# Performance work log

Measured on AMD Instinct MI355X. Metric: run time of the kernel, lower is better.

## Reference

```python
import jax, jax.numpy as jnp
import numpy as np

B, S, D_MODEL, D_K, D_V, H = 2, 2048, 1024, 1024, 1024, 16


def setup_inputs() -> dict:
    key = jax.random.key(0)
    ks = jax.random.split(key, 12)
    s = 0.02
    inp = {
        "queries": jax.random.normal(ks[0], (B, S, D_MODEL), jnp.float32),
        "keys": jax.random.normal(ks[1], (B, S, D_MODEL), jnp.float32),
        "values": jax.random.normal(ks[2], (B, S, D_MODEL), jnp.float32),
        # causal mask: 1 where attention is disallowed (added as -1e9*mask)
        "mask": jnp.triu(jnp.ones((1, 1, S, S), jnp.float32), k=1),
        "Wq": jax.random.normal(ks[3], (D_MODEL, D_K), jnp.float32) * s,
        "bq": jnp.zeros((D_K,), jnp.float32),
        "Wk": jax.random.normal(ks[4], (D_MODEL, D_K), jnp.float32) * s,
        "bk": jnp.zeros((D_K,), jnp.float32),
        "Wv": jax.random.normal(ks[5], (D_MODEL, D_V), jnp.float32) * s,
        "bv": jnp.zeros((D_V,), jnp.float32),
        "Wo": jax.random.normal(ks[6], (D_K, D_MODEL), jnp.float32) * s,
        "bo": jnp.zeros((D_MODEL,), jnp.float32),
    }
    return inp


def _split_heads(x):  # [B,S,D] -> [B,H,S,D/H]
    b, s, d = x.shape
    return x.reshape(b, s, H, d // H).transpose(0, 2, 1, 3)


def reference(queries, keys, values, mask, Wq, bq, Wk, bk, Wv, bv, Wo, bo):
    q = _split_heads(queries @ Wq + bq)   # [B,H,S,hd]
    k = _split_heads(keys @ Wk + bk)
    v = _split_heads(values @ Wv + bv)
    # NOTE: original scales by sqrt(full d_k), not per-head dim (faithful quirk)
    scores = jnp.einsum("bhqd,bhkd->bhqk", q, k) / jnp.sqrt(jnp.float32(D_K))
    scores = scores + (-1e9) * mask
    w = jax.nn.softmax(scores, axis=-1)
    out = jnp.einsum("bhqk,bhkd->bhqd", w, v)        # [B,H,S,hd]
    out = out.transpose(0, 2, 1, 3).reshape(q.shape[0], q.shape[2], D_K)
    return out @ Wo + bo
```

## Files before the change

### kernel.cpp

```cpp
#include <hip/hip_runtime.h>
#include <hip/hip_bf16.h>
#include <cstdint>

typedef __bf16 bf16;
typedef __bf16 bf16x2 __attribute__((ext_vector_type(2)));
typedef __bf16 bf16x4 __attribute__((ext_vector_type(4)));
typedef __bf16 bf16x8 __attribute__((ext_vector_type(8)));
typedef float f32x4 __attribute__((ext_vector_type(4)));
typedef float f32x16 __attribute__((ext_vector_type(16)));
typedef unsigned int u32;

#define B_ 2
#define S_ 2048
#define DM 1024
#define H_ 16
#define HD 64

__device__ __forceinline__ void gload_lds16(const bf16* g, bf16* l) {
  __builtin_amdgcn_global_load_lds((const __attribute__((address_space(1))) void*)g,
                                   (__attribute__((address_space(3))) void*)l,
                                   16, 0, 0);
}

__device__ __forceinline__ u32 cvt_pk_bf16(float lo, float hi) {
  u32 r;
  asm("v_cvt_pk_bf16_f32 %0, %1, %2" : "=v"(r) : "v"(lo), "v"(hi));
  return r;
}

__global__ __launch_bounds__(256) void convert_k(const float* __restrict__ s0,
                                                 const float* __restrict__ s1,
                                                 const float* __restrict__ s2,
                                                 bf16* __restrict__ d0,
                                                 bf16* __restrict__ d1,
                                                 bf16* __restrict__ d2) {
  const float* s = (blockIdx.z == 0) ? s0 : (blockIdx.z == 1) ? s1 : s2;
  bf16* d = (blockIdx.z == 0) ? d0 : (blockIdx.z == 1) ? d1 : d2;
  const size_t i = ((size_t)blockIdx.x * 256 + threadIdx.x) * 8;
  f32x4 a = *(const f32x4*)(s + i);
  f32x4 b = *(const f32x4*)(s + i + 4);
  bf16x8 o;
#pragma unroll
  for (int j = 0; j < 4; j++) { o[j] = (bf16)a[j]; o[j + 4] = (bf16)b[j]; }
  *(bf16x8*)(d + i) = o;
}

__global__ __launch_bounds__(256) void transposeW_k(
    const float* __restrict__ w0, const float* __restrict__ w1,
    const float* __restrict__ w2, const float* __restrict__ w3,
    bf16* __restrict__ t0, bf16* __restrict__ t1,
    bf16* __restrict__ t2, bf16* __restrict__ t3) {
  const float* src = (blockIdx.z == 0) ? w0 : (blockIdx.z == 1) ? w1
                     : (blockIdx.z == 2) ? w2 : w3;
  bf16* dst = (blockIdx.z == 0) ? t0 : (blockIdx.z == 1) ? t1
              : (blockIdx.z == 2) ? t2 : t3;
  __shared__ float tile[32][33];
  const int tx = threadIdx.x, ty = threadIdx.y;
  const int x0 = blockIdx.x * 32, y0 = blockIdx.y * 32;
#pragma unroll
  for (int r = 0; r < 4; r++)
    tile[ty + r * 8][tx] = src[(size_t)(y0 + ty + r * 8) * DM + x0 + tx];
  __syncthreads();
#pragma unroll
  for (int r = 0; r < 4; r++)
    dst[(size_t)(x0 + ty + r * 8) * DM + y0 + tx] = (bf16)tile[tx][ty + r * 8];
}

struct GArgs { const void* A; const bf16* Bt; const float* bias; void* C; };
struct GArgs3 { GArgs g[3]; };

__global__ __launch_bounds__(512, 1) void gemm128_k(GArgs3 args, int M, int N,
                                                    int K) {
  __shared__ __align__(16) bf16 SA_[73728];
  bf16* const SB_ = SA_ + 24576;

  const int nwg = gridDim.x;
  const int id = blockIdx.x;
  const int wgid = (id & 7) * (nwg >> 3) + (id >> 3);
  const int z = wgid >> 7;
  const int rem = wgid & 127;
  const int tx = rem >> 5, ty = rem & 31;
  const GArgs ga = args.g[z];
  const int m0 = ty * 128, n0 = tx * 256;

  const int tid = threadIdx.x;
  const int lane = tid & 63, w = tid >> 6;
  const int l15 = lane & 15, q = lane >> 4;
  const int wr = w >> 2, wc = w & 3;

  const bf16* gA[2];
  const bf16* gB[4];
  int dA[2], dB[4];
#pragma unroll
  for (int i = 0; i < 2; i++) {
    const int ci = i * 512 + w * 64 + lane;
    const int row = ci >> 3, sc = (ci & 7) ^ (row & 7);
    gA[i] = (const bf16*)ga.A + (size_t)(m0 + row) * K + sc * 8;
    dA[i] = (i * 512 + w * 64) * 8;
  }
#pragma unroll
  for (int i = 0; i < 4; i++) {
    const int ci = i * 512 + w * 64 + lane;
    const int row = ci >> 3, sc = (ci & 7) ^ (row & 7);
    gB[i] = ga.Bt + (size_t)(n0 + row) * K + sc * 8;
    dB[i] = (i * 512 + w * 64) * 8;
  }

  const int cA0 = (q ^ (l15 & 7)) * 8;
  const int cA1 = ((4 + q) ^ (l15 & 7)) * 8;

  f32x4 acc[4][4] = {};

  const int NT = K >> 6;

#pragma unroll
  for (int tt = 0; tt < 2; tt++) {
    bf16* Ab = SA_ + tt * 8192;
    bf16* Bb = SB_ + tt * 16384;
    const int k0 = tt * 64;
    gload_lds16(gA[0] + k0, Ab + dA[0]);
    gload_lds16(gA[1] + k0, Ab + dA[1]);
#pragma unroll
    for (int i = 0; i < 4; i++) gload_lds16(gB[i] + k0, Bb + dB[i]);
  }
  asm volatile("s_waitcnt vmcnt(6)" ::: "memory");
  __builtin_amdgcn_s_barrier();

  for (int t = 0; t < NT; ++t) {
    const int rb = t % 3;
    const int wb = (t + 2) % 3;
    const int kpre = ((t + 2 < NT) ? t + 2 : NT - 1) << 6;
    {
      bf16* Ab = SA_ + wb * 8192;
      bf16* Bb = SB_ + wb * 16384;
      gload_lds16(gA[0] + kpre, Ab + dA[0]);
      gload_lds16(gA[1] + kpre, Ab + dA[1]);
#pragma unroll
      for (int i = 0; i < 4; i++) gload_lds16(gB[i] + kpre, Bb + dB[i]);
    }

    const bf16* Ab = SA_ + rb * 8192;
    const bf16* Bb = SB_ + rb * 16384;
    bf16x8 a[4][2], b[4][2];
#pragma unroll
    for (int mt = 0; mt < 4; mt++) {
      const int ro = (wr * 64 + mt * 16 + l15) * 64;
      a[mt][0] = *(const bf16x8*)(Ab + ro + cA0);
      a[mt][1] = *(const bf16x8*)(Ab + ro + cA1);
    }
#pragma unroll
    for (int nt = 0; nt < 4; nt++) {
      const int ro = (wc * 64 + nt * 16 + l15) * 64;
      b[nt][0] = *(const bf16x8*)(Bb + ro + cA0);
      b[nt][1] = *(const bf16x8*)(Bb + ro + cA1);
    }

    __builtin_amdgcn_s_setprio(1);
#pragma unroll
    for (int mt = 0; mt < 4; mt++)
#pragma unroll
      for (int nt = 0; nt < 4; nt++)
#pragma unroll
        for (int kk = 0; kk < 2; kk++)
          acc[mt][nt] = __builtin_amdgcn_mfma_f32_16x16x32_bf16(
              a[mt][kk], b[nt][kk], acc[mt][nt], 0, 0, 0);
    __builtin_amdgcn_s_setprio(0);

    asm volatile("s_waitcnt vmcnt(6)" ::: "memory");
    __builtin_amdgcn_s_barrier();
  }

  asm volatile("s_waitcnt vmcnt(0)" ::: "memory");
  __builtin_amdgcn_s_barrier();

  bf16* Ws = SA_ + w * 4352;
#pragma unroll
  for (int nt = 0; nt < 4; nt++) {
    const float bv = ga.bias[n0 + wc * 64 + nt * 16 + l15];
#pragma unroll
    for (int mt = 0; mt < 4; mt++)
#pragma unroll
      for (int r = 0; r < 4; r++)
        Ws[(mt * 16 + q * 4 + r) * 68 + nt * 16 + l15] =
            (bf16)(acc[mt][nt][r] + bv);
  }
#pragma unroll
  for (int p = 0; p < 8; p++) {
    const int lr = p * 8 + (lane >> 3), c0 = (lane & 7) * 8;
    bf16x4 lo = *(const bf16x4*)(Ws + lr * 68 + c0);
    bf16x4 hi = *(const bf16x4*)(Ws + lr * 68 + c0 + 4);
    bf16x8 o;
#pragma unroll
    for (int j = 0; j < 4; j++) { o[j] = lo[j]; o[j + 4] = hi[j]; }
    *(bf16x8*)((bf16*)ga.C + (size_t)(m0 + wr * 64 + lr) * N + n0 + wc * 64 + c0) = o;
  }
}

template <bool AF32, bool CF32>
__global__ __launch_bounds__(256) void gemm_k(GArgs3 args, int M, int N, int K) {
  const GArgs ga = args.g[blockIdx.z];
  __shared__ __align__(16) bf16 As[128 * 32];
  __shared__ __align__(16) bf16 Bs[128 * 32];
  const int tid = threadIdx.x;
  const int lane = tid & 63, w = tid >> 6;
  const int l15 = lane & 15, q = lane >> 4;
  const int wr = w >> 1, wc = w & 1;

  int bx = blockIdx.x, by = blockIdx.y;
  if constexpr (CF32) {
    const int nb = gridDim.x * gridDim.y;
    const int id = by * gridDim.x + bx;
    const int wg = (id & 7) * (nb >> 3) + (id >> 3);
    bx = wg % gridDim.x;
    by = wg / gridDim.x;
  }
  const int m0 = by * 128, n0 = bx * 128;

  const int c0 = w * 128 + lane;
  const int c1 = c0 + 64;
  const int r0 = c0 >> 2, r1 = c1 >> 2, koff = (c0 & 3) * 8;
  const bf16* gB0 = ga.Bt + (size_t)(n0 + r0) * K + koff;
  const bf16* gB1 = ga.Bt + (size_t)(n0 + r1) * K + koff;
  bf16* lA0 = As + (w * 2 + 0) * 512;
  bf16* lA1 = As + (w * 2 + 1) * 512;
  bf16* lB0 = Bs + (w * 2 + 0) * 512;
  bf16* lB1 = Bs + (w * 2 + 1) * 512;

  const float* pA0 = nullptr;
  const float* pA1 = nullptr;
  f32x4 t00, t01, t10, t11;
  if constexpr (AF32) {
    const float* A = (const float*)ga.A;
    pA0 = A + (size_t)(m0 + r0) * K + koff;
    pA1 = A + (size_t)(m0 + r1) * K + koff;
    t00 = *(const f32x4*)pA0; t01 = *(const f32x4*)(pA0 + 4);
    t10 = *(const f32x4*)pA1; t11 = *(const f32x4*)(pA1 + 4);
  }

  f32x4 acc[4][4] = {};

  for (int k0 = 0; k0 < K; k0 += 32) {
    if constexpr (AF32) {
      bf16x8 va0, va1;
#pragma unroll
      for (int j = 0; j < 4; j++) {
        va0[j] = (bf16)t00[j]; va0[j + 4] = (bf16)t01[j];
        va1[j] = (bf16)t10[j]; va1[j + 4] = (bf16)t11[j];
      }
      *(bf16x8*)(lA0 + lane * 8) = va0;
      *(bf16x8*)(lA1 + lane * 8) = va1;
    } else {
      const bf16* A = (const bf16*)ga.A;
      gload_lds16(A + (size_t)(m0 + r0) * K + koff + k0, lA0);
      gload_lds16(A + (size_t)(m0 + r1) * K + koff + k0, lA1);
    }
    gload_lds16(gB0 + k0, lB0);
    gload_lds16(gB1 + k0, lB1);
    __syncthreads();

    bf16x8 a[4], b[4];
#pragma unroll
    for (int mt = 0; mt < 4; mt++)
      a[mt] = *(const bf16x8*)(As + (wr * 64 + mt * 16 + l15) * 32 + q * 8);
#pragma unroll
    for (int nt = 0; nt < 4; nt++)
      b[nt] = *(const bf16x8*)(Bs + (wc * 64 + nt * 16 + l15) * 32 + q * 8);

    if constexpr (AF32) {
      const int kn = (k0 + 32 < K) ? k0 + 32 : k0;
      t00 = *(const f32x4*)(pA0 + kn); t01 = *(const f32x4*)(pA0 + kn + 4);
      t10 = *(const f32x4*)(pA1 + kn); t11 = *(const f32x4*)(pA1 + kn + 4);
    }

#pragma unroll
    for (int mt = 0; mt < 4; mt++)
#pragma unroll
      for (int nt = 0; nt < 4; nt++)
        acc[mt][nt] = __builtin_amdgcn_mfma_f32_16x16x32_bf16(a[mt], b[nt],
                                                              acc[mt][nt], 0, 0, 0);
    __syncthreads();
  }

#pragma unroll
  for (int nt = 0; nt < 4; nt++) {
    const int col = n0 + wc * 64 + nt * 16 + l15;
    const float bv = ga.bias[col];
#pragma unroll
    for (int mt = 0; mt < 4; mt++) {
      const int row = m0 + wr * 64 + mt * 16 + q * 4;
#pragma unroll
      for (int r = 0; r < 4; r++) {
        const float val = acc[mt][nt][r] + bv;
        if constexpr (CF32)
          ((float*)ga.C)[(size_t)(row + r) * N + col] = val;
        else
          ((bf16*)ga.C)[(size_t)(row + r) * N + col] = (bf16)val;
      }
    }
  }
}

__global__ __launch_bounds__(256, 4) void attn_k(const bf16* __restrict__ Qp,
                                                 const bf16* __restrict__ Kp,
                                                 const bf16* __restrict__ Vp,
                                                 bf16* __restrict__ Op) {
  const int g = blockIdx.x;
  const int xcd = g & 7, s = g >> 3;
  const int gl = s & 3, tau = s >> 2;
  const int bh = xcd * 4 + gl;
  const int b = bh >> 4, h = bh & 15;
  const int o3 = tau & 7, hq = tau >> 3;
  const int xt = (hq == 0) ? o3 : (hq == 1) ? 15 - o3
                 : (hq == 2) ? 16 + o3 : 31 - o3;
  const int i0 = xt * 64;

  const int tid = threadIdx.x;
  const int lane = tid & 63, w = tid >> 6;
  const int l31 = lane & 31, hi = lane >> 5;
  const int qh = w >> 1, kh = w & 1;

  __shared__ __align__(16) char smem[33280];
  bf16 (*Ks)[64][64] = (bf16 (*)[64][64])smem;
  bf16 (*Vts)[64][64] = (bf16 (*)[64][64])(smem + 16384);

  const size_t headoff = (size_t)b * S_ * DM + h * HD;
  const bf16* Kb = Kp + headoff;
  const bf16* Vb = Vp + headoff;

  const int kr0 = tid >> 3, kr1 = 32 + (tid >> 3), kcb = (tid & 7) * 8;
  const int cK = ((tid & 7) ^ (kr0 & 7)) * 8;
  const int d0 = (tid & 31) * 2, kq = (tid >> 5) * 8;
  const int cV0 = ((tid >> 5) ^ (d0 & 7)) * 8;
  const int cV1 = ((tid >> 5) ^ ((d0 + 1) & 7)) * 8;
  const float QSCALE = 0.04508422f;

  bf16x8 qreg[4];
  {
    const bf16* qb = Qp + headoff + (size_t)(i0 + qh * 32 + l31) * DM + hi * 8;
#pragma unroll
    for (int kk = 0; kk < 4; kk++) {
      bf16x8 v = *(const bf16x8*)(qb + kk * 16);
      bf16x8 o;
#pragma unroll
      for (int j = 0; j < 8; j++) o[j] = (bf16)((float)v[j] * QSCALE);
      qreg[kk] = o;
    }
  }

  const int NI = (i0 >> 6) + 1;

  bf16x8 kR0 = *(const bf16x8*)(Kb + (size_t)kr0 * DM + kcb);
  bf16x8 kR1 = *(const bf16x8*)(Kb + (size_t)kr1 * DM + kcb);
  bf16x2 vR[8];
#pragma unroll
  for (int j = 0; j < 8; j++)
    vR[j] = *(const bf16x2*)(Vb + (size_t)(kq + j) * DM + d0);
  *(bf16x8*)&Ks[0][kr0][cK] = kR0;
  *(bf16x8*)&Ks[0][kr1][cK] = kR1;
  {
    bf16x8 vlo, vhi;
#pragma unroll
    for (int j = 0; j < 8; j++) { vlo[j] = vR[j][0]; vhi[j] = vR[j][1]; }
    *(bf16x8*)&Vts[0][d0][cV0] = vlo;
    *(bf16x8*)&Vts[0][d0 + 1][cV1] = vhi;
  }
  if (NI > 1) {
    kR0 = *(const bf16x8*)(Kb + (size_t)(64 + kr0) * DM + kcb);
    kR1 = *(const bf16x8*)(Kb + (size_t)(64 + kr1) * DM + kcb);
#pragma unroll
    for (int j = 0; j < 8; j++)
      vR[j] = *(const bf16x2*)(Vb + (size_t)(64 + kq + j) * DM + d0);
  }
  __syncthreads();

  f32x16 oacc0 = {}, oacc1 = {};
  float rsum = 0.f;
  int buf = 0;

  for (int t = 0; t < NI; ++t, buf ^= 1) {
    if (t + 1 < NI) {
      *(bf16x8*)&Ks[buf ^ 1][kr0][cK] = kR0;
      *(bf16x8*)&Ks[buf ^ 1][kr1][cK] = kR1;
      bf16x8 vlo, vhi;
#pragma unroll
      for (int j = 0; j < 8; j++) { vlo[j] = vR[j][0]; vhi[j] = vR[j][1]; }
      *(bf16x8*)&Vts[buf ^ 1][d0][cV0] = vlo;
      *(bf16x8*)&Vts[buf ^ 1][d0 + 1][cV1] = vhi;
    }
    if (t + 2 < NI) {
      const size_t jn = (size_t)(t + 2) * 64;
      kR0 = *(const bf16x8*)(Kb + (jn + kr0) * DM + kcb);
      kR1 = *(const bf16x8*)(Kb + (jn + kr1) * DM + kcb);
#pragma unroll
      for (int j = 0; j < 8; j++)
        vR[j] = *(const bf16x2*)(Vb + (jn + kq + j) * DM + d0);
    }

    const bool diag = (t == NI - 1);
    if (!(diag && kh > qh)) {
      f32x16 sa = {}, sb = {};
      __builtin_amdgcn_s_setprio(1);
#pragma unroll
      for (int kk = 0; kk < 2; kk++) {
        bf16x8 ka = *(const bf16x8*)
            &Ks[buf][kh * 32 + l31][((2 * kk + hi) ^ (l31 & 7)) * 8];
        sa = __builtin_amdgcn_mfma_f32_32x32x16_bf16(ka, qreg[kk], sa, 0, 0, 0);
      }
#pragma unroll
      for (int kk = 2; kk < 4; kk++) {
        bf16x8 ka = *(const bf16x8*)
            &Ks[buf][kh * 32 + l31][((2 * kk + hi) ^ (l31 & 7)) * 8];
        sb = __builtin_amdgcn_mfma_f32_32x32x16_bf16(ka, qreg[kk], sb, 0, 0, 0);
      }
      __builtin_amdgcn_s_setprio(0);

      float p[16];
      if (diag) {
        const int qrl = qh * 32 + l31;
#pragma unroll
        for (int r = 0; r < 16; r++) {
          const int keyl = kh * 32 + (r & 3) + 8 * (r >> 2) + 4 * hi;
          p[r] = (keyl <= qrl) ? __builtin_amdgcn_exp2f(sa[r] + sb[r]) : 0.f;
        }
      } else {
#pragma unroll
        for (int r = 0; r < 16; r++)
          p[r] = __builtin_amdgcn_exp2f(sa[r] + sb[r]);
      }
      {
        float q0 = (p[0] + p[1]) + (p[2] + p[3]);
        float q1 = (p[4] + p[5]) + (p[6] + p[7]);
        float q2 = (p[8] + p[9]) + (p[10] + p[11]);
        float q3 = (p[12] + p[13]) + (p[14] + p[15]);
        rsum += (q0 + q1) + (q2 + q3);
      }

      u32 Aq[4][2];
#pragma unroll
      for (int t2 = 0; t2 < 4; t2++) {
        Aq[t2][0] = cvt_pk_bf16(p[4 * t2 + 0], p[4 * t2 + 1]);
        Aq[t2][1] = cvt_pk_bf16(p[4 * t2 + 2], p[4 * t2 + 3]);
      }
      bf16x8 pb[2];
#pragma unroll
      for (int s2 = 0; s2 < 2; s2++) {
        auto e0 = __builtin_amdgcn_permlane32_swap(Aq[2 * s2][0], Aq[2 * s2 + 1][0], false, false);
        auto e1 = __builtin_amdgcn_permlane32_swap(Aq[2 * s2][1], Aq[2 * s2 + 1][1], false, false);
        union { u32 u[4]; bf16x8 v; } cv;
        cv.u[0] = e0[0]; cv.u[1] = e1[0]; cv.u[2] = e0[1]; cv.u[3] = e1[1];
        pb[s2] = cv.v;
      }

      __builtin_amdgcn_s_setprio(1);
#pragma unroll
      for (int s2 = 0; s2 < 2; s2++) {
        const int cv = ((kh * 4 + s2 * 2 + hi) ^ (l31 & 7)) * 8;
        bf16x8 va0 = *(const bf16x8*)&Vts[buf][l31][cv];
        bf16x8 va1 = *(const bf16x8*)&Vts[buf][32 + l31][cv];
        oacc0 = __builtin_amdgcn_mfma_f32_32x32x16_bf16(va0, pb[s2], oacc0, 0, 0, 0);
        oacc1 = __builtin_amdgcn_mfma_f32_32x32x16_bf16(va1, pb[s2], oacc1, 0, 0, 0);
      }
      __builtin_amdgcn_s_setprio(0);
    }

    __syncthreads();
  }

  float rtot_w = rsum + __shfl_xor(rsum, 32);
  float* osum = (float*)smem;
  float* auxf = (float*)(smem + 32768);
#pragma unroll
  for (int m = 0; m < 2; m++) {
#pragma unroll
    for (int rq = 0; rq < 4; rq++) {
      f32x4 v4;
#pragma unroll
      for (int e = 0; e < 4; e++)
        v4[e] = m ? oacc1[rq * 4 + e] : oacc0[rq * 4 + e];
      *(f32x4*)(osum + w * 2048 + (m * 4 + rq) * 256 + lane * 4) = v4;
    }
  }
  if (lane < 32) auxf[w * 32 + lane] = rtot_w;
  __syncthreads();

  {
    const int q = tid >> 2, q31b = q & 31, qh2 = q >> 5;
    const float rtot = auxf[(qh2 * 2 + 0) * 32 + q31b] + auxf[(qh2 * 2 + 1) * 32 + q31b];
    const float rinv = 1.0f / rtot;
    const int dbase = (tid & 3) * 16;
    bf16* orow = Op + headoff + (size_t)(i0 + q) * DM + dbase;
#pragma unroll
    for (int gg = 0; gg < 2; gg++) {
      bf16x8 o8;
#pragma unroll
      for (int e = 0; e < 8; e++) {
        const int d = dbase + gg * 8 + e;
        const int base = (((d >> 5) << 2) | ((d >> 3) & 3)) * 256 +
                         (q31b + 32 * ((d >> 2) & 1)) * 4 + (d & 3);
        const float v = osum[(qh2 * 2 + 0) * 2048 + base] +
                        osum[(qh2 * 2 + 1) * 2048 + base];
        o8[e] = (bf16)(v * rinv);
      }
      *(bf16x8*)(orow + gg * 8) = o8;
    }
  }
}

extern "C" void kernel_launch(void* const* d_in, const int* in_sizes, int n_in,
                              void* d_out, int out_size, void* d_ws, size_t ws_size,
                              hipStream_t stream) {
  const float* q_in = (const float*)d_in[0];
  const float* k_in = (const float*)d_in[1];
  const float* v_in = (const float*)d_in[2];
  const float* Wq = (const float*)d_in[4];
  const float* bq = (const float*)d_in[5];
  const float* Wk = (const float*)d_in[6];
  const float* bk = (const float*)d_in[7];
  const float* Wv = (const float*)d_in[8];
  const float* bv = (const float*)d_in[9];
  const float* Wo = (const float*)d_in[10];
  const float* bo = (const float*)d_in[11];

  bf16* ws = (bf16*)d_ws;
  const size_t NQ = (size_t)B_ * S_ * DM;
  bf16* Qp = ws;
  bf16* Kp = ws + NQ;
  bf16* Vp = ws + 2 * NQ;
  bf16* WqT = ws + 3 * NQ;
  bf16* WkT = WqT + (size_t)DM * DM;
  bf16* WvT = WkT + (size_t)DM * DM;
  bf16* WoT = WvT + (size_t)DM * DM;
  bf16* qb = WoT + (size_t)DM * DM;
  bf16* kb = qb + NQ;
  bf16* vb = kb + NQ;

  const bool fast = ws_size >= (size_t)(28 * 1024 * 1024) * 2;

  transposeW_k<<<dim3(32, 32, 4), dim3(32, 8), 0, stream>>>(
      Wq, Wk, Wv, Wo, WqT, WkT, WvT, WoT);

  if (fast) {
    convert_k<<<dim3((B_ * S_ * DM) / (256 * 8), 1, 3), 256, 0, stream>>>(
        q_in, k_in, v_in, qb, kb, vb);
    GArgs3 g3;
    g3.g[0] = {qb, WqT, bq, Qp};
    g3.g[1] = {kb, WkT, bk, Kp};
    g3.g[2] = {vb, WvT, bv, Vp};
    gemm128_k<<<dim3(384), 512, 0, stream>>>(g3, B_ * S_, DM, DM);
  } else {
    GArgs3 g3;
    g3.g[0] = {q_in, WqT, bq, Qp};
    g3.g[1] = {k_in, WkT, bk, Kp};
    g3.g[2] = {v_in, WvT, bv, Vp};
    gemm_k<true, false><<<dim3(DM / 128, (B_ * S_) / 128, 3), 256, 0, stream>>>(
        g3, B_ * S_, DM, DM);
  }

  attn_k<<<dim3(1024, 1, 1), 256, 0, stream>>>(Qp, Kp, Vp, Qp);

  GArgs3 gp;
  gp.g[0] = {Qp, WoT, bo, d_out};
  gp.g[1] = gp.g[0];
  gp.g[2] = gp.g[0];
  gemm_k<false, true><<<dim3(DM / 128, (B_ * S_) / 128, 1), 256, 0, stream>>>(
      gp, B_ * S_, DM, DM);
}
```

Baseline: 227.3 us.

## Shrink QKV GEMM tiles to 128x128 and pair causal query tiles per attention block

The fused QKV projection GEMM moves from 128x256 to 128x128 output tiles. That doubles the grid to 768 workgroups, cuts LDS use, and replaces the LDS-staged vectorized epilogue with direct scalar bf16 stores. The attention kernel now has each block process two query tiles, xt and 31-xt, in sequence, so every block does an equal amount of causal work. The launch is halved to 512 blocks. In exchange, the GEMM stores are strided and uncoalesced and the GEMM reuses data less, and attention has fewer blocks to hide latency.

```diff
diff --git a/kernel.cpp b/kernel.cpp
--- a/kernel.cpp
+++ b/kernel.cpp
@@ -69,19 +69,19 @@
 struct GArgs { const void* A; const bf16* Bt; const float* bias; void* C; };
 struct GArgs3 { GArgs g[3]; };
 
-__global__ __launch_bounds__(512, 1) void gemm128_k(GArgs3 args, int M, int N,
-                                                    int K) {
-  __shared__ __align__(16) bf16 SA_[73728];
+__global__ __launch_bounds__(512, 1) void gemmq_k(GArgs3 args, int M, int N,
+                                                  int K) {
+  __shared__ __align__(16) bf16 SA_[49152];
   bf16* const SB_ = SA_ + 24576;
 
   const int nwg = gridDim.x;
   const int id = blockIdx.x;
   const int wgid = (id & 7) * (nwg >> 3) + (id >> 3);
-  const int z = wgid >> 7;
-  const int rem = wgid & 127;
+  const int z = wgid >> 8;
+  const int rem = wgid & 255;
   const int tx = rem >> 5, ty = rem & 31;
   const GArgs ga = args.g[z];
-  const int m0 = ty * 128, n0 = tx * 256;
+  const int m0 = ty * 128, n0 = tx * 128;
 
   const int tid = threadIdx.x;
   const int lane = tid & 63, w = tid >> 6;
@@ -89,59 +89,46 @@
   const int wr = w >> 2, wc = w & 3;
 
   const bf16* gA[2];
-  const bf16* gB[4];
-  int dA[2], dB[4];
+  const bf16* gB[2];
+  int dd[2];
 #pragma unroll
   for (int i = 0; i < 2; i++) {
     const int ci = i * 512 + w * 64 + lane;
     const int row = ci >> 3, sc = (ci & 7) ^ (row & 7);
     gA[i] = (const bf16*)ga.A + (size_t)(m0 + row) * K + sc * 8;
-    dA[i] = (i * 512 + w * 64) * 8;
-  }
-#pragma unroll
-  for (int i = 0; i < 4; i++) {
-    const int ci = i * 512 + w * 64 + lane;
-    const int row = ci >> 3, sc = (ci & 7) ^ (row & 7);
     gB[i] = ga.Bt + (size_t)(n0 + row) * K + sc * 8;
-    dB[i] = (i * 512 + w * 64) * 8;
+    dd[i] = ci * 8;
   }
 
   const int cA0 = (q ^ (l15 & 7)) * 8;
   const int cA1 = ((4 + q) ^ (l15 & 7)) * 8;
 
-  f32x4 acc[4][4] = {};
-
+  f32x4 acc[4][2] = {};
   const int NT = K >> 6;
 
 #pragma unroll
   for (int tt = 0; tt < 2; tt++) {
-    bf16* Ab = SA_ + tt * 8192;
-    bf16* Bb = SB_ + tt * 16384;
     const int k0 = tt * 64;
-    gload_lds16(gA[0] + k0, Ab + dA[0]);
-    gload_lds16(gA[1] + k0, Ab + dA[1]);
-#pragma unroll
-    for (int i = 0; i < 4; i++) gload_lds16(gB[i] + k0, Bb + dB[i]);
-  }
-  asm volatile("s_waitcnt vmcnt(6)" ::: "memory");
+    gload_lds16(gA[0] + k0, SA_ + tt * 8192 + dd[0]);
+    gload_lds16(gA[1] + k0, SA_ + tt * 8192 + dd[1]);
+    gload_lds16(gB[0] + k0, SB_ + tt * 8192 + dd[0]);
+    gload_lds16(gB[1] + k0, SB_ + tt * 8192 + dd[1]);
+  }
+  asm volatile("s_waitcnt vmcnt(4)" ::: "memory");
   __builtin_amdgcn_s_barrier();
 
   for (int t = 0; t < NT; ++t) {
     const int rb = t % 3;
     const int wb = (t + 2) % 3;
     const int kpre = ((t + 2 < NT) ? t + 2 : NT - 1) << 6;
-    {
-      bf16* Ab = SA_ + wb * 8192;
-      bf16* Bb = SB_ + wb * 16384;
-      gload_lds16(gA[0] + kpre, Ab + dA[0]);
-      gload_lds16(gA[1] + kpre, Ab + dA[1]);
-#pragma unroll
-      for (int i = 0; i < 4; i++) gload_lds16(gB[i] + kpre, Bb + dB[i]);
-    }
+    gload_lds16(gA[0] + kpre, SA_ + wb * 8192 + dd[0]);
+    gload_lds16(gA[1] + kpre, SA_ + wb * 8192 + dd[1]);
+    gload_lds16(gB[0] + kpre, SB_ + wb * 8192 + dd[0]);
+    gload_lds16(gB[1] + kpre, SB_ + wb * 8192 + dd[1]);
 
     const bf16* Ab = SA_ + rb * 8192;
-    const bf16* Bb = SB_ + rb * 16384;
-    bf16x8 a[4][2], b[4][2];
+    const bf16* Bb = SB_ + rb * 8192;
+    bf16x8 a[4][2], b[2][2];
 #pragma unroll
     for (int mt = 0; mt < 4; mt++) {
       const int ro = (wr * 64 + mt * 16 + l15) * 64;
@@ -149,8 +136,8 @@
       a[mt][1] = *(const bf16x8*)(Ab + ro + cA1);
     }
 #pragma unroll
-    for (int nt = 0; nt < 4; nt++) {
-      const int ro = (wc * 64 + nt * 16 + l15) * 64;
+    for (int nt = 0; nt < 2; nt++) {
+      const int ro = (wc * 32 + nt * 16 + l15) * 64;
       b[nt][0] = *(const bf16x8*)(Bb + ro + cA0);
       b[nt][1] = *(const bf16x8*)(Bb + ro + cA1);
     }
@@ -159,40 +146,29 @@
 #pragma unroll
     for (int mt = 0; mt < 4; mt++)
 #pragma unroll
-      for (int nt = 0; nt < 4; nt++)
+      for (int nt = 0; nt < 2; nt++)
 #pragma unroll
         for (int kk = 0; kk < 2; kk++)
           acc[mt][nt] = __builtin_amdgcn_mfma_f32_16x16x32_bf16(
               a[mt][kk], b[nt][kk], acc[mt][nt], 0, 0, 0);
     __builtin_amdgcn_s_setprio(0);
 
-    asm volatile("s_waitcnt vmcnt(6)" ::: "memory");
+    asm volatile("s_waitcnt vmcnt(4)" ::: "memory");
     __builtin_amdgcn_s_barrier();
   }
 
-  asm volatile("s_waitcnt vmcnt(0)" ::: "memory");
-  __builtin_amdgcn_s_barrier();
-
-  bf16* Ws = SA_ + w * 4352;
-#pragma unroll
-  for (int nt = 0; nt < 4; nt++) {
-    const float bv = ga.bias[n0 + wc * 64 + nt * 16 + l15];
-#pragma unroll
-    for (int mt = 0; mt < 4; mt++)
+#pragma unroll
+  for (int nt = 0; nt < 2; nt++) {
+    const int col = n0 + wc * 32 + nt * 16 + l15;
+    const float bv = ga.bias[col];
+#pragma unroll
+    for (int mt = 0; mt < 4; mt++) {
+      const int row = m0 + wr * 64 + mt * 16 + q * 4;
+      f32x4 v = acc[mt][nt];
 #pragma unroll
       for (int r = 0; r < 4; r++)
-        Ws[(mt * 16 + q * 4 + r) * 68 + nt * 16 + l15] =
-            (bf16)(acc[mt][nt][r] + bv);
-  }
-#pragma unroll
-  for (int p = 0; p < 8; p++) {
-    const int lr = p * 8 + (lane >> 3), c0 = (lane & 7) * 8;
-    bf16x4 lo = *(const bf16x4*)(Ws + lr * 68 + c0);
-    bf16x4 hi = *(const bf16x4*)(Ws + lr * 68 + c0 + 4);
-    bf16x8 o;
-#pragma unroll
-    for (int j = 0; j < 4; j++) { o[j] = lo[j]; o[j + 4] = hi[j]; }
-    *(bf16x8*)((bf16*)ga.C + (size_t)(m0 + wr * 64 + lr) * N + n0 + wc * 64 + c0) = o;
+        ((bf16*)ga.C)[(size_t)(row + r) * N + col] = (bf16)(v[r] + bv);
+    }
   }
 }
 
@@ -306,13 +282,9 @@
                                                  bf16* __restrict__ Op) {
   const int g = blockIdx.x;
   const int xcd = g & 7, s = g >> 3;
-  const int gl = s & 3, tau = s >> 2;
+  const int gl = s & 3, pr = s >> 2;
   const int bh = xcd * 4 + gl;
   const int b = bh >> 4, h = bh & 15;
-  const int o3 = tau & 7, hq = tau >> 3;
-  const int xt = (hq == 0) ? o3 : (hq == 1) ? 15 - o3
-                 : (hq == 2) ? 16 + o3 : 31 - o3;
-  const int i0 = xt * 64;
 
   const int tid = threadIdx.x;
   const int lane = tid & 63, w = tid >> 6;
@@ -334,174 +306,181 @@
   const int cV1 = ((tid >> 5) ^ ((d0 + 1) & 7)) * 8;
   const float QSCALE = 0.04508422f;
 
-  bf16x8 qreg[4];
-  {
-    const bf16* qb = Qp + headoff + (size_t)(i0 + qh * 32 + l31) * DM + hi * 8;
-#pragma unroll
-    for (int kk = 0; kk < 4; kk++) {
-      bf16x8 v = *(const bf16x8*)(qb + kk * 16);
-      bf16x8 o;
-#pragma unroll
-      for (int j = 0; j < 8; j++) o[j] = (bf16)((float)v[j] * QSCALE);
-      qreg[kk] = o;
-    }
-  }
-
-  const int NI = (i0 >> 6) + 1;
-
-  bf16x8 kR0 = *(const bf16x8*)(Kb + (size_t)kr0 * DM + kcb);
-  bf16x8 kR1 = *(const bf16x8*)(Kb + (size_t)kr1 * DM + kcb);
-  bf16x2 vR[8];
-#pragma unroll
-  for (int j = 0; j < 8; j++)
-    vR[j] = *(const bf16x2*)(Vb + (size_t)(kq + j) * DM + d0);
-  *(bf16x8*)&Ks[0][kr0][cK] = kR0;
-  *(bf16x8*)&Ks[0][kr1][cK] = kR1;
-  {
-    bf16x8 vlo, vhi;
-#pragma unroll
-    for (int j = 0; j < 8; j++) { vlo[j] = vR[j][0]; vhi[j] = vR[j][1]; }
-    *(bf16x8*)&Vts[0][d0][cV0] = vlo;
-    *(bf16x8*)&Vts[0][d0 + 1][cV1] = vhi;
-  }
-  if (NI > 1) {
-    kR0 = *(const bf16x8*)(Kb + (size_t)(64 + kr0) * DM + kcb);
-    kR1 = *(const bf16x8*)(Kb + (size_t)(64 + kr1) * DM + kcb);
+#pragma unroll 1
+  for (int half = 0; half < 2; half++) {
+    const int xt = half ? pr : 31 - pr;
+    const int i0 = xt * 64;
+    const int NI = xt + 1;
+
+    __syncthreads();
+
+    bf16x8 qreg[4];
+    {
+      const bf16* qb = Qp + headoff + (size_t)(i0 + qh * 32 + l31) * DM + hi * 8;
+#pragma unroll
+      for (int kk = 0; kk < 4; kk++) {
+        bf16x8 v = *(const bf16x8*)(qb + kk * 16);
+        bf16x8 o;
+#pragma unroll
+        for (int j = 0; j < 8; j++) o[j] = (bf16)((float)v[j] * QSCALE);
+        qreg[kk] = o;
+      }
+    }
+
+    bf16x8 kR0 = *(const bf16x8*)(Kb + (size_t)kr0 * DM + kcb);
+    bf16x8 kR1 = *(const bf16x8*)(Kb + (size_t)kr1 * DM + kcb);
+    bf16x2 vR[8];
 #pragma unroll
     for (int j = 0; j < 8; j++)
-      vR[j] = *(const bf16x2*)(Vb + (size_t)(64 + kq + j) * DM + d0);
-  }
-  __syncthreads();
-
-  f32x16 oacc0 = {}, oacc1 = {};
-  float rsum = 0.f;
-  int buf = 0;
-
-  for (int t = 0; t < NI; ++t, buf ^= 1) {
-    if (t + 1 < NI) {
-      *(bf16x8*)&Ks[buf ^ 1][kr0][cK] = kR0;
-      *(bf16x8*)&Ks[buf ^ 1][kr1][cK] = kR1;
+      vR[j] = *(const bf16x2*)(Vb + (size_t)(kq + j) * DM + d0);
+    *(bf16x8*)&Ks[0][kr0][cK] = kR0;
+    *(bf16x8*)&Ks[0][kr1][cK] = kR1;
+    {
       bf16x8 vlo, vhi;
 #pragma unroll
       for (int j = 0; j < 8; j++) { vlo[j] = vR[j][0]; vhi[j] = vR[j][1]; }
-      *(bf16x8*)&Vts[buf ^ 1][d0][cV0] = vlo;
-      *(bf16x8*)&Vts[buf ^ 1][d0 + 1][cV1] = vhi;
-    }
-    if (t + 2 < NI) {
-      const size_t jn = (size_t)(t + 2) * 64;
-      kR0 = *(const bf16x8*)(Kb + (jn + kr0) * DM + kcb);
-      kR1 = *(const bf16x8*)(Kb + (jn + kr1) * DM + kcb);
+      *(bf16x8*)&Vts[0][d0][cV0] = vlo;
+      *(bf16x8*)&Vts[0][d0 + 1][cV1] = vhi;
+    }
+    if (NI > 1) {
+      kR0 = *(const bf16x8*)(Kb + (size_t)(64 + kr0) * DM + kcb);
+      kR1 = *(const bf16x8*)(Kb + (size_t)(64 + kr1) * DM + kcb);
 #pragma unroll
       for (int j = 0; j < 8; j++)
-        vR[j] = *(const bf16x2*)(Vb + (jn + kq + j) * DM + d0);
-    }
-
-    const bool diag = (t == NI - 1);
-    if (!(diag && kh > qh)) {
-      f32x16 sa = {}, sb = {};
-      __builtin_amdgcn_s_setprio(1);
-#pragma unroll
-      for (int kk = 0; kk < 2; kk++) {
-        bf16x8 ka = *(const bf16x8*)
-            &Ks[buf][kh * 32 + l31][((2 * kk + hi) ^ (l31 & 7)) * 8];
-        sa = __builtin_amdgcn_mfma_f32_32x32x16_bf16(ka, qreg[kk], sa, 0, 0, 0);
-      }
-#pragma unroll
-      for (int kk = 2; kk < 4; kk++) {
-        bf16x8 ka = *(const bf16x8*)
-            &Ks[buf][kh * 32 + l31][((2 * kk + hi) ^ (l31 & 7)) * 8];
-        sb = __builtin_amdgcn_mfma_f32_32x32x16_bf16(ka, qreg[kk], sb, 0, 0, 0);
-      }
-      __builtin_amdgcn_s_setprio(0);
-
-      float p[16];
-      if (diag) {
-        const int qrl = qh * 32 + l31;
-#pragma unroll
-        for (int r = 0; r < 16; r++) {
-          const int keyl = kh * 32 + (r & 3) + 8 * (r >> 2) + 4 * hi;
-          p[r] = (keyl <= qrl) ? __builtin_amdgcn_exp2f(sa[r] + sb[r]) : 0.f;
-        }
-      } else {
-#pragma unroll
-        for (int r = 0; r < 16; r++)
-          p[r] = __builtin_amdgcn_exp2f(sa[r] + sb[r]);
-      }
-      {
-        float q0 = (p[0] + p[1]) + (p[2] + p[3]);
-        float q1 = (p[4] + p[5]) + (p[6] + p[7]);
-        float q2 = (p[8] + p[9]) + (p[10] + p[11]);
-        float q3 = (p[12] + p[13]) + (p[14] + p[15]);
-        rsum += (q0 + q1) + (q2 + q3);
-      }
-
-      u32 Aq[4][2];
-#pragma unroll
-      for (int t2 = 0; t2 < 4; t2++) {
-        Aq[t2][0] = cvt_pk_bf16(p[4 * t2 + 0], p[4 * t2 + 1]);
-        Aq[t2][1] = cvt_pk_bf16(p[4 * t2 + 2], p[4 * t2 + 3]);
-      }
-      bf16x8 pb[2];
-#pragma unroll
-      for (int s2 = 0; s2 < 2; s2++) {
-        auto e0 = __builtin_amdgcn_permlane32_swap(Aq[2 * s2][0], Aq[2 * s2 + 1][0], false, false);
-        auto e1 = __builtin_amdgcn_permlane32_swap(Aq[2 * s2][1], Aq[2 * s2 + 1][1], false, false);
-        union { u32 u[4]; bf16x8 v; } cv;
-        cv.u[0] = e0[0]; cv.u[1] = e1[0]; cv.u[2] = e0[1]; cv.u[3] = e1[1];
-        pb[s2] = cv.v;
-      }
-
-      __builtin_amdgcn_s_setprio(1);
-#pragma unroll
-      for (int s2 = 0; s2 < 2; s2++) {
-        const int cv = ((kh * 4 + s2 * 2 + hi) ^ (l31 & 7)) * 8;
-        bf16x8 va0 = *(const bf16x8*)&Vts[buf][l31][cv];
-        bf16x8 va1 = *(const bf16x8*)&Vts[buf][32 + l31][cv];
-        oacc0 = __builtin_amdgcn_mfma_f32_32x32x16_bf16(va0, pb[s2], oacc0, 0, 0, 0);
-        oacc1 = __builtin_amdgcn_mfma_f32_32x32x16_bf16(va1, pb[s2], oacc1, 0, 0, 0);
-      }
-      __builtin_amdgcn_s_setprio(0);
-    }
-
+        vR[j] = *(const bf16x2*)(Vb + (size_t)(64 + kq + j) * DM + d0);
+    }
     __syncthreads();
-  }
-
-  float rtot_w = rsum + __shfl_xor(rsum, 32);
-  float* osum = (float*)smem;
-  float* auxf = (float*)(smem + 32768);
-#pragma unroll
-  for (int m = 0; m < 2; m++) {
-#pragma unroll
-    for (int rq = 0; rq < 4; rq++) {
-      f32x4 v4;
-#pragma unroll
-      for (int e = 0; e < 4; e++)
-        v4[e] = m ? oacc1[rq * 4 + e] : oacc0[rq * 4 + e];
-      *(f32x4*)(osum + w * 2048 + (m * 4 + rq) * 256 + lane * 4) = v4;
-    }
-  }
-  if (lane < 32) auxf[w * 32 + lane] = rtot_w;
-  __syncthreads();
-
-  {
-    const int q = tid >> 2, q31b = q & 31, qh2 = q >> 5;
-    const float rtot = auxf[(qh2 * 2 + 0) * 32 + q31b] + auxf[(qh2 * 2 + 1) * 32 + q31b];
-    const float rinv = 1.0f / rtot;
-    const int dbase = (tid & 3) * 16;
-    bf16* orow = Op + headoff + (size_t)(i0 + q) * DM + dbase;
-#pragma unroll
-    for (int gg = 0; gg < 2; gg++) {
-      bf16x8 o8;
-#pragma unroll
-      for (int e = 0; e < 8; e++) {
-        const int d = dbase + gg * 8 + e;
-        const int base = (((d >> 5) << 2) | ((d >> 3) & 3)) * 256 +
-                         (q31b + 32 * ((d >> 2) & 1)) * 4 + (d & 3);
-        const float v = osum[(qh2 * 2 + 0) * 2048 + base] +
-                        osum[(qh2 * 2 + 1) * 2048 + base];
-        o8[e] = (bf16)(v * rinv);
-      }
-      *(bf16x8*)(orow + gg * 8) = o8;
+
+    f32x16 oacc0 = {}, oacc1 = {};
+    float rsum = 0.f;
+    int buf = 0;
+
+    for (int t = 0; t < NI; ++t, buf ^= 1) {
+      if (t + 1 < NI) {
+        *(bf16x8*)&Ks[buf ^ 1][kr0][cK] = kR0;
+        *(bf16x8*)&Ks[buf ^ 1][kr1][cK] = kR1;
+        bf16x8 vlo, vhi;
+#pragma unroll
+        for (int j = 0; j < 8; j++) { vlo[j] = vR[j][0]; vhi[j] = vR[j][1]; }
+        *(bf16x8*)&Vts[buf ^ 1][d0][cV0] = vlo;
+        *(bf16x8*)&Vts[buf ^ 1][d0 + 1][cV1] = vhi;
+      }
+      if (t + 2 < NI) {
+        const size_t jn = (size_t)(t + 2) * 64;
+        kR0 = *(const bf16x8*)(Kb + (jn + kr0) * DM + kcb);
+        kR1 = *(const bf16x8*)(Kb + (jn + kr1) * DM + kcb);
+#pragma unroll
+        for (int j = 0; j < 8; j++)
+          vR[j] = *(const bf16x2*)(Vb + (jn + kq + j) * DM + d0);
+      }
+
+      const bool diag = (t == NI - 1);
+      if (!(diag && kh > qh)) {
+        f32x16 sa = {}, sb = {};
+        __builtin_amdgcn_s_setprio(1);
+#pragma unroll
+        for (int kk = 0; kk < 2; kk++) {
+          bf16x8 ka = *(const bf16x8*)
+              &Ks[buf][kh * 32 + l31][((2 * kk + hi) ^ (l31 & 7)) * 8];
+          sa = __builtin_amdgcn_mfma_f32_32x32x16_bf16(ka, qreg[kk], sa, 0, 0, 0);
+        }
+#pragma unroll
+        for (int kk = 2; kk < 4; kk++) {
+          bf16x8 ka = *(const bf16x8*)
+              &Ks[buf][kh * 32 + l31][((2 * kk + hi) ^ (l31 & 7)) * 8];
+          sb = __builtin_amdgcn_mfma_f32_32x32x16_bf16(ka, qreg[kk], sb, 0, 0, 0);
+        }
+        __builtin_amdgcn_s_setprio(0);
+
+        float p[16];
+        if (diag) {
+          const int qrl = qh * 32 + l31;
+#pragma unroll
+          for (int r = 0; r < 16; r++) {
+            const int keyl = kh * 32 + (r & 3) + 8 * (r >> 2) + 4 * hi;
+            p[r] = (keyl <= qrl) ? __builtin_amdgcn_exp2f(sa[r] + sb[r]) : 0.f;
+          }
+        } else {
+#pragma unroll
+          for (int r = 0; r < 16; r++)
+            p[r] = __builtin_amdgcn_exp2f(sa[r] + sb[r]);
+        }
+        {
+          float q0 = (p[0] + p[1]) + (p[2] + p[3]);
+          float q1 = (p[4] + p[5]) + (p[6] + p[7]);
+          float q2 = (p[8] + p[9]) + (p[10] + p[11]);
+          float q3 = (p[12] + p[13]) + (p[14] + p[15]);
+          rsum += (q0 + q1) + (q2 + q3);
+        }
+
+        u32 Aq[4][2];
+#pragma unroll
+        for (int t2 = 0; t2 < 4; t2++) {
+          Aq[t2][0] = cvt_pk_bf16(p[4 * t2 + 0], p[4 * t2 + 1]);
+          Aq[t2][1] = cvt_pk_bf16(p[4 * t2 + 2], p[4 * t2 + 3]);
+        }
+        bf16x8 pb[2];
+#pragma unroll
+        for (int s2 = 0; s2 < 2; s2++) {
+          auto e0 = __builtin_amdgcn_permlane32_swap(Aq[2 * s2][0], Aq[2 * s2 + 1][0], false, false);
+          auto e1 = __builtin_amdgcn_permlane32_swap(Aq[2 * s2][1], Aq[2 * s2 + 1][1], false, false);
+          union { u32 u[4]; bf16x8 v; } cv;
+          cv.u[0] = e0[0]; cv.u[1] = e1[0]; cv.u[2] = e0[1]; cv.u[3] = e1[1];
+          pb[s2] = cv.v;
+        }
+
+        __builtin_amdgcn_s_setprio(1);
+#pragma unroll
+        for (int s2 = 0; s2 < 2; s2++) {
+          const int cv = ((kh * 4 + s2 * 2 + hi) ^ (l31 & 7)) * 8;
+          bf16x8 va0 = *(const bf16x8*)&Vts[buf][l31][cv];
+          bf16x8 va1 = *(const bf16x8*)&Vts[buf][32 + l31][cv];
+          oacc0 = __builtin_amdgcn_mfma_f32_32x32x16_bf16(va0, pb[s2], oacc0, 0, 0, 0);
+          oacc1 = __builtin_amdgcn_mfma_f32_32x32x16_bf16(va1, pb[s2], oacc1, 0, 0, 0);
+        }
+        __builtin_amdgcn_s_setprio(0);
+      }
+
+      __syncthreads();
+    }
+
+    float rtot_w = rsum + __shfl_xor(rsum, 32);
+    float* osum = (float*)smem;
+    float* auxf = (float*)(smem + 32768);
+#pragma unroll
+    for (int m = 0; m < 2; m++) {
+#pragma unroll
+      for (int rq = 0; rq < 4; rq++) {
+        f32x4 v4;
+#pragma unroll
+        for (int e = 0; e < 4; e++)
+          v4[e] = m ? oacc1[rq * 4 + e] : oacc0[rq * 4 + e];
+        *(f32x4*)(osum + w * 2048 + (m * 4 + rq) * 256 + lane * 4) = v4;
+      }
+    }
+    if (lane < 32) auxf[w * 32 + lane] = rtot_w;
+    __syncthreads();
+
+    {
+      const int q = tid >> 2, q31b = q & 31, qh2 = q >> 5;
+      const float rtot = auxf[(qh2 * 2 + 0) * 32 + q31b] + auxf[(qh2 * 2 + 1) * 32 + q31b];
+      const float rinv = 1.0f / rtot;
+      const int dbase = (tid & 3) * 16;
+      bf16* orow = Op + headoff + (size_t)(i0 + q) * DM + dbase;
+#pragma unroll
+      for (int gg = 0; gg < 2; gg++) {
+        bf16x8 o8;
+#pragma unroll
+        for (int e = 0; e < 8; e++) {
+          const int d = dbase + gg * 8 + e;
+          const int base = (((d >> 5) << 2) | ((d >> 3) & 3)) * 256 +
+                           (q31b + 32 * ((d >> 2) & 1)) * 4 + (d & 3);
+          const float v = osum[(qh2 * 2 + 0) * 2048 + base] +
+                          osum[(qh2 * 2 + 1) * 2048 + base];
+          o8[e] = (bf16)(v * rinv);
+        }
+        *(bf16x8*)(orow + gg * 8) = o8;
+      }
     }
   }
 }
@@ -546,7 +525,7 @@
     g3.g[0] = {qb, WqT, bq, Qp};
     g3.g[1] = {kb, WkT, bk, Kp};
     g3.g[2] = {vb, WvT, bv, Vp};
-    gemm128_k<<<dim3(384), 512, 0, stream>>>(g3, B_ * S_, DM, DM);
+    gemmq_k<<<dim3(768), 512, 0, stream>>>(g3, B_ * S_, DM, DM);
   } else {
     GArgs3 g3;
     g3.g[0] = {q_in, WqT, bq, Qp};
@@ -556,7 +535,7 @@
         g3, B_ * S_, DM, DM);
   }
 
-  attn_k<<<dim3(1024, 1, 1), 256, 0, stream>>>(Qp, Kp, Vp, Qp);
+  attn_k<<<dim3(512, 1, 1), 256, 0, stream>>>(Qp, Kp, Vp, Qp);
 
   GArgs3 gp;
   gp.g[0] = {Qp, WoT, bo, d_out};
```

Result: slower. 248.0 us (+9.1%).

## Add dedicated output-projection GEMM with triple-buffered async LDS pipeline

Applied to the files above, without the earlier changes.

Replaces the generic 256-thread gemm_k used for the output projection with a new 512-thread kernel. It uses 64-wide K tiles, XOR-swizzled LDS layout, direct global-to-LDS loads in a 3-stage ring buffer, and a wider 16x16x32 bf16 MFMA. The goal is to hide memory latency and reduce bank conflicts for the final fp32-output GEMM, and the XCD-aware block remapping moves into the new kernel. It uses about 96KB of LDS and allows one workgroup per CU, so occupancy is lower.

```diff
diff --git a/kernel.cpp b/kernel.cpp
--- a/kernel.cpp
+++ b/kernel.cpp
@@ -196,6 +196,114 @@
   }
 }
 
+__global__ __launch_bounds__(512, 1) void gemmo_k(const bf16* __restrict__ A,
+                                                  const bf16* __restrict__ Bt,
+                                                  const float* __restrict__ bias,
+                                                  float* __restrict__ C,
+                                                  int M, int N, int K) {
+  __shared__ __align__(16) bf16 SA_[49152];
+  bf16* const SB_ = SA_ + 24576;
+
+  const int id = blockIdx.x;
+  const int wgid = (id & 7) * 32 + (id >> 3);
+  const int tx = wgid >> 5, ty = wgid & 31;
+  const int m0 = ty * 128, n0 = tx * 128;
+
+  const int tid = threadIdx.x;
+  const int lane = tid & 63, w = tid >> 6;
+  const int l15 = lane & 15, q = lane >> 4;
+  const int wr = w >> 2, wc = w & 3;
+
+  const bf16* gA[2];
+  const bf16* gB[2];
+  int dd[2];
+#pragma unroll
+  for (int i = 0; i < 2; i++) {
+    const int ci = i * 512 + w * 64 + lane;
+    const int row = ci >> 3, sc = (ci & 7) ^ (row & 7);
+    gA[i] = A + (size_t)(m0 + row) * K + sc * 8;
+    gB[i] = Bt + (size_t)(n0 + row) * K + sc * 8;
+    dd[i] = ci * 8;
+  }
+
+  const int cA0 = (q ^ (l15 & 7)) * 8;
+  const int cA1 = ((4 + q) ^ (l15 & 7)) * 8;
+
+  f32x4 acc[4][2] = {};
+  const int NT = K >> 6;
+
+#pragma unroll
+  for (int tt = 0; tt < 2; tt++) {
+    const int k0 = tt * 64;
+    gload_lds16(gA[0] + k0, SA_ + tt * 8192 + dd[0]);
+    gload_lds16(gA[1] + k0, SA_ + tt * 8192 + dd[1]);
+    gload_lds16(gB[0] + k0, SB_ + tt * 8192 + dd[0]);
+    gload_lds16(gB[1] + k0, SB_ + tt * 8192 + dd[1]);
+  }
+  asm volatile("s_waitcnt vmcnt(4)" ::: "memory");
+  __builtin_amdgcn_s_barrier();
+
+  for (int t = 0; t < NT; ++t) {
+    const int rb = t % 3;
+    const int wb = (t + 2) % 3;
+    const int kpre = ((t + 2 < NT) ? t + 2 : NT - 1) << 6;
+    gload_lds16(gA[0] + kpre, SA_ + wb * 8192 + dd[0]);
+    gload_lds16(gA[1] + kpre, SA_ + wb * 8192 + dd[1]);
+    gload_lds16(gB[0] + kpre, SB_ + wb * 8192 + dd[0]);
+    gload_lds16(gB[1] + kpre, SB_ + wb * 8192 + dd[1]);
+
+    const bf16* Ab = SA_ + rb * 8192;
+    const bf16* Bb = SB_ + rb * 8192;
+    bf16x8 a[4][2], b[2][2];
+#pragma unroll
+    for (int mt = 0; mt < 4; mt++) {
+      const int ro = (wr * 64 + mt * 16 + l15) * 64;
+      a[mt][0] = *(const bf16x8*)(Ab + ro + cA0);
+      a[mt][1] = *(const bf16x8*)(Ab + ro + cA1);
+    }
+#pragma unroll
+    for (int nt = 0; nt < 2; nt++) {
+      const int ro = (wc * 32 + nt * 16 + l15) * 64;
+      b[nt][0] = *(const bf16x8*)(Bb + ro + cA0);
+      b[nt][1] = *(const bf16x8*)(Bb + ro + cA1);
+    }
+
+    __builtin_amdgcn_s_setprio(1);
+#pragma unroll
+    for (int mt = 0; mt < 4; mt++)
+#pragma unroll
+      for (int nt = 0; nt < 2; nt++)
+#pragma unroll
+        for (int kk = 0; kk < 2; kk++)
+          acc[mt][nt] = __builtin_amdgcn_mfma_f32_16x16x32_bf16(
+              a[mt][kk], b[nt][kk], acc[mt][nt], 0, 0, 0);
+    __builtin_amdgcn_s_setprio(0);
+
+    asm volatile("s_waitcnt vmcnt(4)" ::: "memory");
+    __builtin_amdgcn_s_barrier();
+  }
+
+  asm volatile("s_waitcnt vmcnt(0)" ::: "memory");
+  __builtin_amdgcn_s_barrier();
+
+  float* Ws = (float*)SA_ + w * 2304;
+#pragma unroll
+  for (int nt = 0; nt < 2; nt++) {
+    const float bv = bias[n0 + wc * 32 + nt * 16 + l15];
+#pragma unroll
+    for (int mt = 0; mt < 4; mt++)
+#pragma unroll
+      for (int r = 0; r < 4; r++)
+        Ws[(mt * 16 + q * 4 + r) * 36 + nt * 16 + l15] = acc[mt][nt][r] + bv;
+  }
+#pragma unroll
+  for (int p = 0; p < 8; p++) {
+    const int lr = p * 8 + (lane >> 3), c0 = (lane & 7) * 4;
+    f32x4 v = *(const f32x4*)(Ws + lr * 36 + c0);
+    *(f32x4*)(C + (size_t)(m0 + wr * 64 + lr) * N + n0 + wc * 32 + c0) = v;
+  }
+}
+
 template <bool AF32, bool CF32>
 __global__ __launch_bounds__(256) void gemm_k(GArgs3 args, int M, int N, int K) {
   const GArgs ga = args.g[blockIdx.z];
@@ -205,16 +313,7 @@
   const int lane = tid & 63, w = tid >> 6;
   const int l15 = lane & 15, q = lane >> 4;
   const int wr = w >> 1, wc = w & 1;
-
-  int bx = blockIdx.x, by = blockIdx.y;
-  if constexpr (CF32) {
-    const int nb = gridDim.x * gridDim.y;
-    const int id = by * gridDim.x + bx;
-    const int wg = (id & 7) * (nb >> 3) + (id >> 3);
-    bx = wg % gridDim.x;
-    by = wg / gridDim.x;
-  }
-  const int m0 = by * 128, n0 = bx * 128;
+  const int m0 = blockIdx.y * 128, n0 = blockIdx.x * 128;
 
   const int c0 = w * 128 + lane;
   const int c1 = c0 + 64;
@@ -558,10 +657,6 @@
 
   attn_k<<<dim3(1024, 1, 1), 256, 0, stream>>>(Qp, Kp, Vp, Qp);
 
-  GArgs3 gp;
-  gp.g[0] = {Qp, WoT, bo, d_out};
-  gp.g[1] = gp.g[0];
-  gp.g[2] = gp.g[0];
-  gemm_k<false, true><<<dim3(DM / 128, (B_ * S_) / 128, 1), 256, 0, stream>>>(
-      gp, B_ * S_, DM, DM);
-}
+  gemmo_k<<<dim3(256), 512, 0, stream>>>(Qp, WoT, bo, (float*)d_out,
+                                         B_ * S_, DM, DM);
+}
```

Measured after the change: 221.0 us. 2.7% less time.
